# Performance work log

Measured on AMD Instinct MI355X. Metric: run time of the kernel, lower is better.

The kernel has to match this reference:

```python
import jax, jax.numpy as jnp
import numpy as np

B0 = 4
DIM = 128        # d_model / channels
D_INNER = 256    # expand * dim
D_STATE = 16
D_CONV = 4
DT_RANK = 8      # ceil(dim/16)
NSLICES = 16
IMG = (16, 24, 24)
EPS_LN = 1e-5    # nn.LayerNorm default
EPS_CF = 1e-6    # channels_first LayerNorm eps


def setup_inputs() -> dict:
    key = jax.random.key(0)
    ks = jax.random.split(key, 32)
    rn = lambda k, s, sc=1.0: jax.random.normal(k, s, jnp.float32) * sc
    inp = {"x": rn(ks[0], (B0, DIM) + IMG)}
    inp["ln_w"] = jnp.ones((DIM,), jnp.float32)
    inp["ln_b"] = jnp.zeros((DIM,), jnp.float32)
    inp["in_proj_w"] = rn(ks[1], (2 * D_INNER, DIM), 0.05)
    inp["out_proj_w"] = rn(ks[2], (DIM, D_INNER), 0.05)
    for i, sfx in enumerate(["f", "b", "s"]):
        b = 3 + i * 7
        inp[f"conv_w_{sfx}"] = rn(ks[b], (D_INNER, 1, D_CONV), 0.2)
        inp[f"conv_b_{sfx}"] = rn(ks[b + 1], (D_INNER,), 0.02)
        inp[f"xproj_w_{sfx}"] = rn(ks[b + 2], (DT_RANK + 2 * D_STATE, D_INNER), 0.05)
        inp[f"dtproj_w_{sfx}"] = rn(ks[b + 3], (D_INNER, DT_RANK), 0.1)
        inp[f"dtproj_b_{sfx}"] = rn(ks[b + 4], (D_INNER,), 0.1)
        # S4D-real-style init: A in [1, d_state]
        inp[f"A_log_{sfx}"] = jnp.log(jax.random.uniform(ks[b + 5], (D_INNER, D_STATE), jnp.float32, 1.0, 16.0))
        inp[f"D_{sfx}"] = jnp.ones((D_INNER,), jnp.float32)
    inp["nm_w"] = jnp.ones((DIM,), jnp.float32)
    inp["nm_b"] = jnp.zeros((DIM,), jnp.float32)
    return inp


def _mamba_inner(xz, conv_w, conv_b, xproj_w, dtproj_w, dtproj_b, A_log, Dp):
    """mamba_inner_fn_no_out_proj: xz (B, 2*d_inner, L) -> y (B, d_inner, L)."""
    d = conv_w.shape[0]
    x, z = xz[:, :d], xz[:, d:]
    # causal depthwise conv1d
    xc = jax.lax.conv_general_dilated(
        x, conv_w, (1,), [(conv_w.shape[-1] - 1, 0)],
        dimension_numbers=("NCH", "OIH", "NCH"), feature_group_count=d)
    xc = jax.nn.silu(xc + conv_b[None, :, None])
    x_dbl = jnp.einsum("bdl,rd->brl", xc, xproj_w)  # (B, R+2N, L)
    R = dtproj_w.shape[1]
    N = A_log.shape[1]
    dt = jax.nn.softplus(jnp.einsum("brl,dr->bdl", x_dbl[:, :R], dtproj_w) + dtproj_b[None, :, None])
    Bm, Cm = x_dbl[:, R:R + N], x_dbl[:, R + N:]
    A = -jnp.exp(A_log)  # (d, N)
    seq = (jnp.moveaxis(dt, -1, 0), jnp.moveaxis(xc, -1, 0),
           jnp.moveaxis(Bm, -1, 0), jnp.moveaxis(Cm, -1, 0))
    h0 = jnp.zeros((xz.shape[0], d, N), xz.dtype)

    def step(h, t):
        dt_t, u_t, B_t, C_t = t  # (B,d) (B,d) (B,N) (B,N)
        h = h * jnp.exp(dt_t[..., None] * A) + (dt_t * u_t)[..., None] * B_t[:, None, :]
        return h, jnp.einsum("bdn,bn->bd", h, C_t)

    _, ys = jax.lax.scan(step, h0, seq)  # ys: (L, B, d)
    y = jnp.moveaxis(ys, 0, -1) + Dp[None, :, None] * xc
    return y * jax.nn.silu(z)


def reference(x, ln_w, ln_b, in_proj_w, out_proj_w,
              conv_w_f, conv_b_f, xproj_w_f, dtproj_w_f, dtproj_b_f, A_log_f, D_f,
              conv_w_b, conv_b_b, xproj_w_b, dtproj_w_b, dtproj_b_b, A_log_b, D_b,
              conv_w_s, conv_b_s, xproj_w_s, dtproj_w_s, dtproj_b_s, A_log_s, D_s,
              nm_w, nm_b):
    B, C = x.shape[:2]
    img = x.shape[2:]
    L = int(np.prod(img))
    xf = jnp.transpose(x.reshape(B, C, L), (0, 2, 1))  # (B, L, C)
    # MambaLayer.norm (nn.LayerNorm over C)
    mu = xf.mean(-1, keepdims=True)
    var = ((xf - mu) ** 2).mean(-1, keepdims=True)
    xn = (xf - mu) / jnp.sqrt(var + EPS_LN) * ln_w + ln_b
    xz = jnp.einsum("blc,ec->bel", xn, in_proj_w)  # (B, 2*d_inner, L)
    # forward-direction scan
    out_f = _mamba_inner(xz, conv_w_f, conv_b_f, xproj_w_f, dtproj_w_f, dtproj_b_f, A_log_f, D_f)
    # backward-direction scan on flipped sequence, flipped back
    out_bw = jnp.flip(_mamba_inner(jnp.flip(xz, -1), conv_w_b, conv_b_b, xproj_w_b,
                                   dtproj_w_b, dtproj_b_b, A_log_b, D_b), -1)
    # slice-direction: torch chunk(nslices,-1) -> stack(-1) -> flatten(-2)
    ns, Lns = NSLICES, L // NSLICES
    xz_s = jnp.transpose(xz.reshape(B, 2 * D_INNER, ns, Lns), (0, 1, 3, 2)).reshape(B, 2 * D_INNER, L)
    out_s = _mamba_inner(xz_s, conv_w_s, conv_b_s, xproj_w_s, dtproj_w_s, dtproj_b_s, A_log_s, D_s)
    # torch: reshape(B,-1,ns,L//ns).permute(0,1,3,2).flatten(-2)
    out_s = jnp.transpose(out_s.reshape(B, D_INNER, ns, Lns), (0, 1, 3, 2)).reshape(B, D_INNER, L)
    y = jnp.einsum("bdl,cd->blc", out_f + out_bw + out_s, out_proj_w)  # out_proj, no bias
    x_mamba = jnp.transpose(y, (0, 2, 1)).reshape(x.shape) + x  # MambaLayer residual
    # SMBBlock: channels_first LayerNorm + residual
    mu2 = x_mamba.mean(1, keepdims=True)
    var2 = ((x_mamba - mu2) ** 2).mean(1, keepdims=True)
    bc = (C,) + (1,) * len(img)
    normed = nm_w.reshape(bc) * ((x_mamba - mu2) / jnp.sqrt(var2 + EPS_CF)) + nm_b.reshape(bc)
    return x_mamba + normed
```

## Files before the change

kernel.cpp:

```cpp
#include <hip/hip_runtime.h>

#define LSEQ 9216
#define CDIM 128
#define ED   512
#define DI   256
#define NST  16
#define NCH  512
#define CHL  18
#define SEG  32
#define LOG2E 1.44269504f
#define LN2  0.6931471805599453f

#if defined(__has_builtin)
#  if __has_builtin(__builtin_amdgcn_exp2f)
#    define FEXP2(x) __builtin_amdgcn_exp2f(x)
#  endif
#  if __has_builtin(__builtin_amdgcn_logf)
#    define FLOG2(x) __builtin_amdgcn_logf(x)
#  endif
#  if __has_builtin(__builtin_amdgcn_rcpf)
#    define FRCP(x) __builtin_amdgcn_rcpf(x)
#  endif
#endif
#ifndef FEXP2
#  define FEXP2(x) exp2f(x)
#endif
#ifndef FLOG2
#  define FLOG2(x) log2f(x)
#endif
#ifndef FRCP
#  define FRCP(x) (1.f / (x))
#endif

typedef __attribute__((ext_vector_type(8))) short short8v;
typedef __attribute__((ext_vector_type(4))) float float4v;

__device__ __forceinline__ float fsilu(float x) {
  return x * FRCP(1.f + FEXP2(-LOG2E * x));
}
__device__ __forceinline__ float fsoftplus(float x) {
  float sp = FLOG2(1.f + FEXP2(LOG2E * x)) * LN2;
  return (x > 20.f) ? x : sp;
}
__device__ __forceinline__ unsigned short f2bf(float f) {
  union { float f; unsigned u; } v; v.f = f;
  return (unsigned short)((v.u + 0x7FFFu + ((v.u >> 16) & 1u)) >> 16);
}
__device__ __forceinline__ float bf2f(unsigned short u) {
  union { unsigned u; float f; } v; v.u = ((unsigned)u) << 16;
  return v.f;
}
__device__ __forceinline__ int lmap(int p, int mode) {
  if (mode == 0) return p;
  if (mode == 1) return LSEQ - 1 - p;
  return (p & 15) * 576 + (p >> 4);
}

__global__ __launch_bounds__(256) void a2_kernel(
    const float* __restrict__ Af, const float* __restrict__ Ab,
    const float* __restrict__ As, float* __restrict__ A2) {
  int i = blockIdx.x * 256 + threadIdx.x;
  if (i >= 3 * DI * NST) return;
  int dir = i / (DI * NST), j = i % (DI * NST);
  const float* src = (dir == 0) ? Af : ((dir == 1) ? Ab : As);
  A2[i] = -expf(src[j]) * LOG2E;
}

__global__ __launch_bounds__(256) void wcast_kernel(
    const float* __restrict__ src, unsigned short* __restrict__ dst, int n) {
  int i = blockIdx.x * 256 + threadIdx.x;
  if (i < n) dst[i] = f2bf(src[i]);
}

__global__ __launch_bounds__(256) void ln_kernel(
    const float* __restrict__ x, const float* __restrict__ w,
    const float* __restrict__ bb, unsigned short* __restrict__ xn) {
  __shared__ float xt[CDIM][65];
  __shared__ float ps[4][64], pq[4][64];
  __shared__ float mu_s[64], rs_s[64];
  const int b = blockIdx.y, l0 = blockIdx.x * 64, tid = threadIdx.x;
  for (int idx = tid; idx < CDIM * 64; idx += 256) {
    int c = idx >> 6, ll = idx & 63;
    xt[c][ll] = x[((size_t)(b * CDIM + c)) * LSEQ + l0 + ll];
  }
  __syncthreads();
  {
    int ll = tid & 63, grp = tid >> 6;
    float s = 0.f, q = 0.f;
    for (int c = grp * 32; c < grp * 32 + 32; ++c) {
      float v = xt[c][ll]; s += v; q += v * v;
    }
    ps[grp][ll] = s; pq[grp][ll] = q;
  }
  __syncthreads();
  if (tid < 64) {
    float S = ps[0][tid] + ps[1][tid] + ps[2][tid] + ps[3][tid];
    float Q = pq[0][tid] + pq[1][tid] + pq[2][tid] + pq[3][tid];
    float mu = S * (1.f / 128.f);
    float var = Q * (1.f / 128.f) - mu * mu;
    mu_s[tid] = mu;
    rs_s[tid] = rsqrtf(var + 1e-5f);
  }
  __syncthreads();
  for (int idx = tid; idx < 64 * CDIM; idx += 256) {
    int c = idx & 127, ll = idx >> 7;
    float v = (xt[c][ll] - mu_s[ll]) * rs_s[ll] * w[c] + bb[c];
    xn[((size_t)(b * LSEQ + l0 + ll)) * CDIM + c] = f2bf(v);
  }
}

template <bool A_BF16, bool OUT_BF16>
__global__ __launch_bounds__(256) void gemm_mfma(
    const void* __restrict__ Ap, const unsigned short* __restrict__ Wb,
    void* __restrict__ Outp, int N, int K, int ldo) {
  __shared__ __align__(16) unsigned short As[64][40];
  __shared__ __align__(16) unsigned short Bs[128][40];
  const int tid = threadIdx.x;
  const int lane = tid & 63, wid = tid >> 6;
  const int wr = wid >> 1, wc = wid & 1;
  const int m0 = blockIdx.x * 64, n0 = blockIdx.y * 128;
  float4v acc[2][4];
#pragma unroll
  for (int s = 0; s < 2; ++s)
#pragma unroll
    for (int t = 0; t < 4; ++t)
#pragma unroll
      for (int r = 0; r < 4; ++r) acc[s][t][r] = 0.f;

  const int srow = tid >> 2, sslot = tid & 3;
  for (int k0 = 0; k0 < K; k0 += 32) {
    if constexpr (A_BF16) {
      const unsigned short* A = (const unsigned short*)Ap;
      *(short8v*)&As[srow][sslot * 8] =
          *(const short8v*)&A[(size_t)(m0 + srow) * K + k0 + sslot * 8];
    } else {
      const float* A = (const float*)Ap;
      const float4* src = (const float4*)&A[(size_t)(m0 + srow) * K + k0 + sslot * 8];
      float4 f0 = src[0], f1 = src[1];
      short8v v;
      v[0] = (short)f2bf(f0.x); v[1] = (short)f2bf(f0.y);
      v[2] = (short)f2bf(f0.z); v[3] = (short)f2bf(f0.w);
      v[4] = (short)f2bf(f1.x); v[5] = (short)f2bf(f1.y);
      v[6] = (short)f2bf(f1.z); v[7] = (short)f2bf(f1.w);
      *(short8v*)&As[srow][sslot * 8] = v;
    }
#pragma unroll
    for (int i = 0; i < 2; ++i) {
      int row = i * 64 + srow;
      int n = n0 + row;
      short8v v;
      if (n < N) {
        v = *(const short8v*)&Wb[(size_t)n * K + k0 + sslot * 8];
      } else {
#pragma unroll
        for (int q = 0; q < 8; ++q) v[q] = 0;
      }
      *(short8v*)&Bs[row][sslot * 8] = v;
    }
    __syncthreads();
    const int kk = (lane >> 4) * 8;
    const int mr = wr * 32 + (lane & 15);
    const int nr = wc * 64 + (lane & 15);
    short8v a_frag[2], b_frag[4];
#pragma unroll
    for (int s = 0; s < 2; ++s)
      a_frag[s] = *(const short8v*)&As[mr + s * 16][kk];
#pragma unroll
    for (int t = 0; t < 4; ++t)
      b_frag[t] = *(const short8v*)&Bs[nr + t * 16][kk];
#pragma unroll
    for (int s = 0; s < 2; ++s)
#pragma unroll
      for (int t = 0; t < 4; ++t)
        acc[s][t] = __builtin_amdgcn_mfma_f32_16x16x32_bf16(
            a_frag[s], b_frag[t], acc[s][t], 0, 0, 0);
    __syncthreads();
  }
  const int rbase = (lane >> 4) * 4;
  const int cbase = lane & 15;
#pragma unroll
  for (int s = 0; s < 2; ++s)
#pragma unroll
    for (int t = 0; t < 4; ++t) {
      int n = n0 + wc * 64 + t * 16 + cbase;
      if (n < N) {
#pragma unroll
        for (int r = 0; r < 4; ++r) {
          int m = m0 + wr * 32 + s * 16 + rbase + r;
          if constexpr (OUT_BF16)
            ((unsigned short*)Outp)[(size_t)m * ldo + n] = f2bf(acc[s][t][r]);
          else
            ((float*)Outp)[(size_t)m * ldo + n] = acc[s][t][r];
        }
      }
    }
}

__global__ __launch_bounds__(256) void gemm_out_final(
    const unsigned short* __restrict__ yf, const unsigned short* __restrict__ yb,
    const unsigned short* __restrict__ ys, const unsigned short* __restrict__ Wb,
    const float* __restrict__ x, const float* __restrict__ nmw,
    const float* __restrict__ nmb, float* __restrict__ out) {
  __shared__ __align__(16) unsigned short As[64][40];
  __shared__ __align__(16) unsigned short Bs[128][40];
  __shared__ float yt[64][129];
  __shared__ float ps[4][64], pq[4][64], mu_s[64], rs_s[64];
  const int tid = threadIdx.x;
  const int lane = tid & 63, wid = tid >> 6;
  const int wr = wid >> 1, wc = wid & 1;
  const int m0 = blockIdx.x * 64;
  const int b = blockIdx.x / 144, l0 = (blockIdx.x % 144) * 64;
  float4v acc[2][4];
#pragma unroll
  for (int s = 0; s < 2; ++s)
#pragma unroll
    for (int t = 0; t < 4; ++t)
#pragma unroll
      for (int r = 0; r < 4; ++r) acc[s][t][r] = 0.f;

  const int srow = tid >> 2, sslot = tid & 3;
  for (int k0 = 0; k0 < 256; k0 += 32) {
    {
      size_t base = (size_t)(m0 + srow) * DI + k0 + sslot * 8;
      short8v vf = *(const short8v*)&yf[base];
      short8v vb = *(const short8v*)&yb[base];
      short8v vs = *(const short8v*)&ys[base];
      short8v v;
#pragma unroll
      for (int q = 0; q < 8; ++q) {
        float f = bf2f((unsigned short)vf[q]) + bf2f((unsigned short)vb[q]) +
                  bf2f((unsigned short)vs[q]);
        v[q] = (short)f2bf(f);
      }
      *(short8v*)&As[srow][sslot * 8] = v;
    }
#pragma unroll
    for (int i = 0; i < 2; ++i) {
      int row = i * 64 + srow;
      *(short8v*)&Bs[row][sslot * 8] =
          *(const short8v*)&Wb[(size_t)row * 256 + k0 + sslot * 8];
    }
    __syncthreads();
    const int kk = (lane >> 4) * 8;
    const int mr = wr * 32 + (lane & 15);
    const int nr = wc * 64 + (lane & 15);
    short8v a_frag[2], b_frag[4];
#pragma unroll
    for (int s = 0; s < 2; ++s)
      a_frag[s] = *(const short8v*)&As[mr + s * 16][kk];
#pragma unroll
    for (int t = 0; t < 4; ++t)
      b_frag[t] = *(const short8v*)&Bs[nr + t * 16][kk];
#pragma unroll
    for (int s = 0; s < 2; ++s)
#pragma unroll
      for (int t = 0; t < 4; ++t)
        acc[s][t] = __builtin_amdgcn_mfma_f32_16x16x32_bf16(
            a_frag[s], b_frag[t], acc[s][t], 0, 0, 0);
    __syncthreads();
  }
  const int rbase = (lane >> 4) * 4;
  const int cbase = lane & 15;
#pragma unroll
  for (int s = 0; s < 2; ++s)
#pragma unroll
    for (int t = 0; t < 4; ++t) {
      int cc = wc * 64 + t * 16 + cbase;
#pragma unroll
      for (int r = 0; r < 4; ++r)
        yt[wr * 32 + s * 16 + rbase + r][cc] = acc[s][t][r];
    }
  __syncthreads();
  for (int idx = tid; idx < CDIM * 64; idx += 256) {
    int c = idx >> 6, ll = idx & 63;
    yt[ll][c] += x[((size_t)(b * CDIM + c)) * LSEQ + l0 + ll];
  }
  __syncthreads();
  {
    int ll = tid & 63, grp = tid >> 6;
    float s = 0.f, q = 0.f;
    for (int c = grp * 32; c < grp * 32 + 32; ++c) {
      float v = yt[ll][c]; s += v; q += v * v;
    }
    ps[grp][ll] = s; pq[grp][ll] = q;
  }
  __syncthreads();
  if (tid < 64) {
    float S = ps[0][tid] + ps[1][tid] + ps[2][tid] + ps[3][tid];
    float Q = pq[0][tid] + pq[1][tid] + pq[2][tid] + pq[3][tid];
    float mu = S * (1.f / 128.f);
    float var = Q * (1.f / 128.f) - mu * mu;
    mu_s[tid] = mu;
    rs_s[tid] = rsqrtf(var + 1e-6f);
  }
  __syncthreads();
  for (int idx = tid; idx < CDIM * 64; idx += 256) {
    int c = idx >> 6, ll = idx & 63;
    float v = yt[ll][c];
    out[((size_t)(b * CDIM + c)) * LSEQ + l0 + ll] =
        v + nmw[c] * (v - mu_s[ll]) * rs_s[ll] + nmb[c];
  }
}

template <int MODE>
__global__ __launch_bounds__(256) void conv_kernel(
    const unsigned short* __restrict__ xz, const float* __restrict__ cw,
    const float* __restrict__ cb, unsigned short* __restrict__ xc) {
  __shared__ float xs[67][64];
  const int p0 = blockIdx.x * 64, d0 = blockIdx.y * 64, b = blockIdx.z;
  const int tid = threadIdx.x;
  for (int idx = tid; idx < 67 * 32; idx += 256) {
    int pp = idx >> 5, dd2 = idx & 31;
    int q = p0 + pp - 3;
    float v0 = 0.f, v1 = 0.f;
    if (q >= 0) {
      int l = lmap(q, MODE);
      unsigned uu = *(const unsigned*)&xz[((size_t)b * LSEQ + l) * ED + d0 + dd2 * 2];
      union { unsigned u; float f; } a, c;
      a.u = (uu & 0xFFFFu) << 16;
      c.u = uu & 0xFFFF0000u;
      v0 = a.f; v1 = c.f;
    }
    xs[pp][dd2 * 2] = v0;
    xs[pp][dd2 * 2 + 1] = v1;
  }
  __syncthreads();
  const int dd = tid & 63, pg = tid >> 6;
  const int d = d0 + dd;
  const float w0 = cw[d * 4 + 0], w1 = cw[d * 4 + 1];
  const float w2 = cw[d * 4 + 2], w3 = cw[d * 4 + 3];
  const float bias = cb[d];
  for (int pp = pg * 16; pp < pg * 16 + 16; ++pp) {
    float acc = bias + w0 * xs[pp][dd] + w1 * xs[pp + 1][dd] +
                w2 * xs[pp + 2][dd] + w3 * xs[pp + 3][dd];
    xc[((size_t)b * LSEQ + p0 + pp) * DI + d] = f2bf(fsilu(acc));
  }
}

__global__ __launch_bounds__(256, 8) void scan_p1(
    const unsigned short* __restrict__ xc, const float* __restrict__ xdbl,
    const float* __restrict__ A2, const float* __restrict__ dtw,
    const float* __restrict__ dtbias, unsigned short* __restrict__ hout,
    float* __restrict__ dts) {
  __shared__ __align__(16) float Xl[CHL][24];
  const int c = blockIdx.x, b = blockIdx.y, d = threadIdx.x;
  const int p0 = c * CHL;
  for (int idx = d; idx < CHL * 24; idx += 256) {
    int pr = idx / 24, r = idx % 24;
    Xl[pr][r] = xdbl[((size_t)b * LSEQ + p0 + pr) * 40 + r];
  }
  float a2[NST], h[NST], dw[8];
  {
    const float4* A2v = (const float4*)(A2 + d * NST);
#pragma unroll
    for (int q = 0; q < 4; ++q) {
      float4 t = A2v[q];
      a2[q * 4 + 0] = t.x; a2[q * 4 + 1] = t.y;
      a2[q * 4 + 2] = t.z; a2[q * 4 + 3] = t.w;
    }
    const float4* Wv = (const float4*)(dtw + d * 8);
    float4 w0 = Wv[0], w1 = Wv[1];
    dw[0] = w0.x; dw[1] = w0.y; dw[2] = w0.z; dw[3] = w0.w;
    dw[4] = w1.x; dw[5] = w1.y; dw[6] = w1.z; dw[7] = w1.w;
  }
#pragma unroll
  for (int n = 0; n < NST; ++n) h[n] = 0.f;
  const float dbias = dtbias[d];
  float dtsum = 0.f;
  const unsigned short* up = xc + ((size_t)b * LSEQ + p0) * DI + d;
  __syncthreads();
  for (int pr = 0; pr < CHL; ++pr) {
    const float u = bf2f(*up); up += DI;
    const float4* Xr = (const float4*)Xl[pr];
    float4 x0 = Xr[0], x1 = Xr[1];
    float raw = dbias;
    raw = fmaf(dw[0], x0.x, raw); raw = fmaf(dw[1], x0.y, raw);
    raw = fmaf(dw[2], x0.z, raw); raw = fmaf(dw[3], x0.w, raw);
    raw = fmaf(dw[4], x1.x, raw); raw = fmaf(dw[5], x1.y, raw);
    raw = fmaf(dw[6], x1.z, raw); raw = fmaf(dw[7], x1.w, raw);
    const float dtv = fsoftplus(raw);
    const float dtu = dtv * u;
    dtsum += dtv;
    float4 b0 = Xr[2], b1 = Xr[3], b2 = Xr[4], b3 = Xr[5];
    const float Bv[16] = {b0.x, b0.y, b0.z, b0.w, b1.x, b1.y, b1.z, b1.w,
                          b2.x, b2.y, b2.z, b2.w, b3.x, b3.y, b3.z, b3.w};
#pragma unroll
    for (int n = 0; n < NST; ++n) {
      float a = FEXP2(dtv * a2[n]);
      h[n] = fmaf(h[n], a, dtu * Bv[n]);
    }
  }
  unsigned short* hb = hout + (((size_t)c * 4 + b) * DI + d) * NST;
  uint4 pk0, pk1;
  pk0.x = ((unsigned)f2bf(h[1]) << 16) | f2bf(h[0]);
  pk0.y = ((unsigned)f2bf(h[3]) << 16) | f2bf(h[2]);
  pk0.z = ((unsigned)f2bf(h[5]) << 16) | f2bf(h[4]);
  pk0.w = ((unsigned)f2bf(h[7]) << 16) | f2bf(h[6]);
  pk1.x = ((unsigned)f2bf(h[9]) << 16) | f2bf(h[8]);
  pk1.y = ((unsigned)f2bf(h[11]) << 16) | f2bf(h[10]);
  pk1.z = ((unsigned)f2bf(h[13]) << 16) | f2bf(h[12]);
  pk1.w = ((unsigned)f2bf(h[15]) << 16) | f2bf(h[14]);
  *(uint4*)hb = pk0;
  *(uint4*)(hb + 8) = pk1;
  dts[((size_t)c * 4 + b) * DI + d] = dtsum;
}

__global__ __launch_bounds__(256) void scan_p2a(
    unsigned short* __restrict__ hbuf, const float* __restrict__ dts,
    const float* __restrict__ A2, float* __restrict__ cumdts,
    float* __restrict__ segH, float* __restrict__ segdts) {
  const int s = blockIdx.x >> 4;
  const int rest = ((blockIdx.x & 15) << 8) + threadIdx.x;
  const int b = blockIdx.y;
  const int d = rest >> 4;
  const float a2 = A2[rest];
  const int c0 = s * SEG;
  float h = 0.f, cum = 0.f;
  float nh = bf2f(hbuf[((size_t)(c0 * 4 + b) << 12) + rest]);
  float nd = dts[(size_t)(c0 * 4 + b) * DI + d];
  for (int c = c0; c < c0 + SEG; ++c) {
    const float tmp = nh, dcur = nd;
    if (c + 1 < c0 + SEG) {
      nh = bf2f(hbuf[((size_t)((c + 1) * 4 + b) << 12) + rest]);
      nd = dts[(size_t)((c + 1) * 4 + b) * DI + d];
    }
    if ((rest & 15) == 0) cumdts[(size_t)(c * 4 + b) * DI + d] = cum;
    cum += dcur;
    hbuf[((size_t)(c * 4 + b) << 12) + rest] = f2bf(h);
    h = fmaf(FEXP2(dcur * a2), h, tmp);
  }
  segH[((size_t)(s * 4 + b) << 12) + rest] = h;
  if ((rest & 15) == 0) segdts[(size_t)(s * 4 + b) * DI + d] = cum;
}

__global__ __launch_bounds__(256) void scan_p2b(
    const float* __restrict__ segH, const float* __restrict__ segdts,
    const float* __restrict__ A2, float* __restrict__ segcarry) {
  const int g = blockIdx.x * 256 + threadIdx.x;
  const int b = g >> 12;
  const int rest = g & 4095;
  const int d = rest >> 4;
  const float a2 = A2[rest];
  float carry = 0.f;
#pragma unroll
  for (int s = 0; s < 16; ++s) {
    segcarry[((size_t)(s * 4 + b) << 12) + rest] = carry;
    const float decay = FEXP2(segdts[(size_t)(s * 4 + b) * DI + d] * a2);
    carry = fmaf(decay, carry, segH[((size_t)(s * 4 + b) << 12) + rest]);
  }
}

template <int MODE>
__global__ __launch_bounds__(256, 8) void scan_p3(
    const unsigned short* __restrict__ xc, const float* __restrict__ xdbl,
    const unsigned short* __restrict__ xz, const float* __restrict__ A2,
    const float* __restrict__ dtw, const float* __restrict__ dtbias,
    const unsigned short* __restrict__ hinit, const float* __restrict__ cumdts,
    const float* __restrict__ segcarry, const float* __restrict__ Dp,
    unsigned short* __restrict__ ybuf) {
  __shared__ __align__(16) float Xl[CHL][40];
  const int c = blockIdx.x, b = blockIdx.y, d = threadIdx.x;
  const int p0 = c * CHL;
  for (int idx = d; idx < CHL * 40; idx += 256) {
    int pr = idx / 40, r = idx % 40;
    Xl[pr][r] = xdbl[((size_t)b * LSEQ + p0 + pr) * 40 + r];
  }
  float a2[NST], h[NST], dw[8];
  {
    const float4* A2v = (const float4*)(A2 + d * NST);
#pragma unroll
    for (int q = 0; q < 4; ++q) {
      float4 t = A2v[q];
      a2[q * 4 + 0] = t.x; a2[q * 4 + 1] = t.y;
      a2[q * 4 + 2] = t.z; a2[q * 4 + 3] = t.w;
    }
    const uint4* Hv = (const uint4*)(hinit + (((size_t)c * 4 + b) * DI + d) * NST);
    uint4 pa = Hv[0], pb = Hv[1];
    const unsigned pw[8] = {pa.x, pa.y, pa.z, pa.w, pb.x, pb.y, pb.z, pb.w};
#pragma unroll
    for (int j = 0; j < 8; ++j) {
      union { unsigned u; float f; } lo, hi;
      lo.u = (pw[j] & 0xFFFFu) << 16;
      hi.u = pw[j] & 0xFFFF0000u;
      h[2 * j] = lo.f; h[2 * j + 1] = hi.f;
    }
    const float cum = cumdts[((size_t)c * 4 + b) * DI + d];
    const float4* SC = (const float4*)(segcarry +
        (((size_t)(c / SEG) * 4 + b) << 12) + d * NST);
#pragma unroll
    for (int q = 0; q < 4; ++q) {
      float4 sc = SC[q];
      const float scv[4] = {sc.x, sc.y, sc.z, sc.w};
#pragma unroll
      for (int r = 0; r < 4; ++r) {
        int n = q * 4 + r;
        h[n] = fmaf(FEXP2(a2[n] * cum), scv[r], h[n]);
      }
    }
    const float4* Wv = (const float4*)(dtw + d * 8);
    float4 w0 = Wv[0], w1 = Wv[1];
    dw[0] = w0.x; dw[1] = w0.y; dw[2] = w0.z; dw[3] = w0.w;
    dw[4] = w1.x; dw[5] = w1.y; dw[6] = w1.z; dw[7] = w1.w;
  }
  const float dbias = dtbias[d];
  const float Dv = Dp[d];

  const unsigned short* up = xc + ((size_t)b * LSEQ + p0) * DI + d;
  const unsigned short* zp;
  unsigned short* op;
  ptrdiff_t zstride, ostride;
  if (MODE == 0) {
    zp = xz + ((size_t)b * LSEQ + p0) * ED + DI + d;              zstride = ED;
    op = ybuf + ((size_t)b * LSEQ + p0) * DI + d;                 ostride = DI;
  } else if (MODE == 1) {
    zp = xz + ((size_t)b * LSEQ + (LSEQ - 1 - p0)) * ED + DI + d; zstride = -(ptrdiff_t)ED;
    op = ybuf + ((size_t)b * LSEQ + (LSEQ - 1 - p0)) * DI + d;    ostride = -(ptrdiff_t)DI;
  } else {
    zp = nullptr; zstride = 0;
    const int lo0 = (p0 % 576) * 16 + p0 / 576;
    op = ybuf + ((size_t)b * LSEQ + lo0) * DI + d;                ostride = 16 * DI;
  }
  __syncthreads();
  for (int pr = 0; pr < CHL; ++pr) {
    const float u = bf2f(*up); up += DI;
    const float4* Xr = (const float4*)Xl[pr];
    float4 x0 = Xr[0], x1 = Xr[1];
    float raw = dbias;
    raw = fmaf(dw[0], x0.x, raw); raw = fmaf(dw[1], x0.y, raw);
    raw = fmaf(dw[2], x0.z, raw); raw = fmaf(dw[3], x0.w, raw);
    raw = fmaf(dw[4], x1.x, raw); raw = fmaf(dw[5], x1.y, raw);
    raw = fmaf(dw[6], x1.z, raw); raw = fmaf(dw[7], x1.w, raw);
    const float dtv = fsoftplus(raw);
    const float dtu = dtv * u;
    float4 b0 = Xr[2], b1 = Xr[3], b2 = Xr[4], b3 = Xr[5];
    float4 c0 = Xr[6], c1 = Xr[7], c2 = Xr[8], c3 = Xr[9];
    const float Bv[16] = {b0.x, b0.y, b0.z, b0.w, b1.x, b1.y, b1.z, b1.w,
                          b2.x, b2.y, b2.z, b2.w, b3.x, b3.y, b3.z, b3.w};
    const float Cv[16] = {c0.x, c0.y, c0.z, c0.w, c1.x, c1.y, c1.z, c1.w,
                          c2.x, c2.y, c2.z, c2.w, c3.x, c3.y, c3.z, c3.w};
    float y0 = Dv * u, y1 = 0.f;
#pragma unroll
    for (int n = 0; n < NST; ++n) {
      float a = FEXP2(dtv * a2[n]);
      h[n] = fmaf(h[n], a, dtu * Bv[n]);
      if (n & 1) y1 = fmaf(h[n], Cv[n], y1);
      else       y0 = fmaf(h[n], Cv[n], y0);
    }
    float z;
    if (MODE == 2) {
      const int p = p0 + pr;
      const int lz = (p & 15) * 576 + (p >> 4);
      z = bf2f(xz[((size_t)b * LSEQ + lz) * ED + DI + d]);
    } else {
      z = bf2f(*zp); zp += zstride;
    }
    *op = f2bf((y0 + y1) * fsilu(z));
    op += ostride;
  }
}

extern "C" void kernel_launch(void* const* d_in, const int* in_sizes, int n_in,
                              void* d_out, int out_size, void* d_ws, size_t ws_size,
                              hipStream_t stream) {
  (void)in_sizes; (void)n_in; (void)out_size;
  const float* x         = (const float*)d_in[0];
  const float* ln_w      = (const float*)d_in[1];
  const float* ln_b      = (const float*)d_in[2];
  const float* in_proj_w = (const float*)d_in[3];
  const float* out_projw = (const float*)d_in[4];
  const float* conv_w[3] = {(const float*)d_in[5],  (const float*)d_in[12], (const float*)d_in[19]};
  const float* conv_b[3] = {(const float*)d_in[6],  (const float*)d_in[13], (const float*)d_in[20]};
  const float* xproj[3]  = {(const float*)d_in[7],  (const float*)d_in[14], (const float*)d_in[21]};
  const float* dtw[3]    = {(const float*)d_in[8],  (const float*)d_in[15], (const float*)d_in[22]};
  const float* dtb[3]    = {(const float*)d_in[9],  (const float*)d_in[16], (const float*)d_in[23]};
  const float* alog[3]   = {(const float*)d_in[10], (const float*)d_in[17], (const float*)d_in[24]};
  const float* Dvec[3]   = {(const float*)d_in[11], (const float*)d_in[18], (const float*)d_in[25]};
  const float* nm_w      = (const float*)d_in[26];
  const float* nm_b      = (const float*)d_in[27];

  float* ws = (float*)d_ws;
  unsigned short* xn_us   = (unsigned short*)(ws);
  unsigned short* xz_us   = (unsigned short*)(ws + 2359296);
  unsigned short* xc_us   = (unsigned short*)(ws + 11796480);
  float* xdbl   = ws + 16515072;
  unsigned short* yf_us   = (unsigned short*)(ws + 17989632);
  unsigned short* yb_us   = (unsigned short*)(ws + 22708224);
  unsigned short* ys_us   = (unsigned short*)(ws + 27426816);
  float* A2     = ws + 32145408;
  unsigned short* wb = (unsigned short*)(ws + 32157696);
  unsigned short* hout_us = (unsigned short*)(ws + 32223232);
  float* dts      = ws + 36417536;
  float* cumdts   = ws + 36941824;
  float* segH     = ws + 37466112;
  float* segdts   = ws + 37728256;
  float* segcarry = ws + 37744640;
  if (ws_size < (size_t)38006784 * sizeof(float)) return;

  unsigned short* wb_in  = wb;
  unsigned short* wb_xp0 = wb + 65536;
  unsigned short* wb_xp1 = wb + 75776;
  unsigned short* wb_xp2 = wb + 86016;
  unsigned short* wb_out = wb + 96256;
  unsigned short* wb_xp[3] = {wb_xp0, wb_xp1, wb_xp2};
  unsigned short* ybuf[3] = {yf_us, yb_us, ys_us};

  a2_kernel<<<48, 256, 0, stream>>>(alog[0], alog[1], alog[2], A2);
  wcast_kernel<<<256, 256, 0, stream>>>(in_proj_w, wb_in, 65536);
  wcast_kernel<<<40, 256, 0, stream>>>(xproj[0], wb_xp0, 10240);
  wcast_kernel<<<40, 256, 0, stream>>>(xproj[1], wb_xp1, 10240);
  wcast_kernel<<<40, 256, 0, stream>>>(xproj[2], wb_xp2, 10240);
  wcast_kernel<<<128, 256, 0, stream>>>(out_projw, wb_out, 32768);

  ln_kernel<<<dim3(LSEQ / 64, 4), 256, 0, stream>>>(x, ln_w, ln_b, xn_us);
  gemm_mfma<true, true><<<dim3(576, 4), 256, 0, stream>>>(xn_us, wb_in, xz_us, 512, 128, 512);

  for (int dir = 0; dir < 3; ++dir) {
    if (dir == 0)
      conv_kernel<0><<<dim3(LSEQ / 64, 4, 4), 256, 0, stream>>>(xz_us, conv_w[0], conv_b[0], xc_us);
    else if (dir == 1)
      conv_kernel<1><<<dim3(LSEQ / 64, 4, 4), 256, 0, stream>>>(xz_us, conv_w[1], conv_b[1], xc_us);
    else
      conv_kernel<2><<<dim3(LSEQ / 64, 4, 4), 256, 0, stream>>>(xz_us, conv_w[2], conv_b[2], xc_us);

    gemm_mfma<true, false><<<dim3(576, 1), 256, 0, stream>>>(xc_us, wb_xp[dir], xdbl, 40, 256, 40);

    const float* A2d = A2 + dir * 4096;
    dim3 sg(NCH, 4);
    scan_p1<<<sg, 256, 0, stream>>>(xc_us, xdbl, A2d, dtw[dir], dtb[dir], hout_us, dts);
    scan_p2a<<<dim3(256, 4), 256, 0, stream>>>(hout_us, dts, A2d, cumdts, segH, segdts);
    scan_p2b<<<64, 256, 0, stream>>>(segH, segdts, A2d, segcarry);

    if (dir == 0)
      scan_p3<0><<<sg, 256, 0, stream>>>(xc_us, xdbl, xz_us, A2d, dtw[0], dtb[0],
                                         hout_us, cumdts, segcarry, Dvec[0], ybuf[0]);
    else if (dir == 1)
      scan_p3<1><<<sg, 256, 0, stream>>>(xc_us, xdbl, xz_us, A2d, dtw[1], dtb[1],
                                         hout_us, cumdts, segcarry, Dvec[1], ybuf[1]);
    else
      scan_p3<2><<<sg, 256, 0, stream>>>(xc_us, xdbl, xz_us, A2d, dtw[2], dtb[2],
                                         hout_us, cumdts, segcarry, Dvec[2], ybuf[2]);
  }
  gemm_out_final<<<576, 256, 0, stream>>>(yf_us, yb_us, ys_us, wb_out, x,
                                          nm_w, nm_b, (float*)d_out);
}
```

Measured before the change: 442.4 us.

## Split scan state dimension across two threads per channel in scan kernels

```diff
diff --git a/kernel.cpp b/kernel.cpp
--- a/kernel.cpp
+++ b/kernel.cpp
@@ -343,28 +343,27 @@
     const float* __restrict__ dtbias, unsigned short* __restrict__ hout,
     float* __restrict__ dts) {
   __shared__ __align__(16) float Xl[CHL][24];
-  const int c = blockIdx.x, b = blockIdx.y, d = threadIdx.x;
+  const int c = blockIdx.x, b = blockIdx.y;
+  const int d = (blockIdx.z << 7) + (threadIdx.x >> 1);
+  const int s = threadIdx.x & 1;
   const int p0 = c * CHL;
-  for (int idx = d; idx < CHL * 24; idx += 256) {
+  for (int idx = threadIdx.x; idx < CHL * 24; idx += 256) {
     int pr = idx / 24, r = idx % 24;
     Xl[pr][r] = xdbl[((size_t)b * LSEQ + p0 + pr) * 40 + r];
   }
-  float a2[NST], h[NST], dw[8];
+  float a2[8], h[8], dw[8];
   {
-    const float4* A2v = (const float4*)(A2 + d * NST);
-#pragma unroll
-    for (int q = 0; q < 4; ++q) {
-      float4 t = A2v[q];
-      a2[q * 4 + 0] = t.x; a2[q * 4 + 1] = t.y;
-      a2[q * 4 + 2] = t.z; a2[q * 4 + 3] = t.w;
-    }
+    const float4* A2v = (const float4*)(A2 + d * NST + s * 8);
+    float4 t0 = A2v[0], t1 = A2v[1];
+    a2[0] = t0.x; a2[1] = t0.y; a2[2] = t0.z; a2[3] = t0.w;
+    a2[4] = t1.x; a2[5] = t1.y; a2[6] = t1.z; a2[7] = t1.w;
     const float4* Wv = (const float4*)(dtw + d * 8);
     float4 w0 = Wv[0], w1 = Wv[1];
     dw[0] = w0.x; dw[1] = w0.y; dw[2] = w0.z; dw[3] = w0.w;
     dw[4] = w1.x; dw[5] = w1.y; dw[6] = w1.z; dw[7] = w1.w;
   }
 #pragma unroll
-  for (int n = 0; n < NST; ++n) h[n] = 0.f;
+  for (int n = 0; n < 8; ++n) h[n] = 0.f;
   const float dbias = dtbias[d];
   float dtsum = 0.f;
   const unsigned short* up = xc + ((size_t)b * LSEQ + p0) * DI + d;
@@ -381,28 +380,22 @@
     const float dtv = fsoftplus(raw);
     const float dtu = dtv * u;
     dtsum += dtv;
-    float4 b0 = Xr[2], b1 = Xr[3], b2 = Xr[4], b3 = Xr[5];
-    const float Bv[16] = {b0.x, b0.y, b0.z, b0.w, b1.x, b1.y, b1.z, b1.w,
-                          b2.x, b2.y, b2.z, b2.w, b3.x, b3.y, b3.z, b3.w};
-#pragma unroll
-    for (int n = 0; n < NST; ++n) {
+    float4 b0 = Xr[2 + 2 * s], b1 = Xr[3 + 2 * s];
+    const float Bv[8] = {b0.x, b0.y, b0.z, b0.w, b1.x, b1.y, b1.z, b1.w};
+#pragma unroll
+    for (int n = 0; n < 8; ++n) {
       float a = FEXP2(dtv * a2[n]);
       h[n] = fmaf(h[n], a, dtu * Bv[n]);
     }
   }
-  unsigned short* hb = hout + (((size_t)c * 4 + b) * DI + d) * NST;
-  uint4 pk0, pk1;
-  pk0.x = ((unsigned)f2bf(h[1]) << 16) | f2bf(h[0]);
-  pk0.y = ((unsigned)f2bf(h[3]) << 16) | f2bf(h[2]);
-  pk0.z = ((unsigned)f2bf(h[5]) << 16) | f2bf(h[4]);
-  pk0.w = ((unsigned)f2bf(h[7]) << 16) | f2bf(h[6]);
-  pk1.x = ((unsigned)f2bf(h[9]) << 16) | f2bf(h[8]);
-  pk1.y = ((unsigned)f2bf(h[11]) << 16) | f2bf(h[10]);
-  pk1.z = ((unsigned)f2bf(h[13]) << 16) | f2bf(h[12]);
-  pk1.w = ((unsigned)f2bf(h[15]) << 16) | f2bf(h[14]);
-  *(uint4*)hb = pk0;
-  *(uint4*)(hb + 8) = pk1;
-  dts[((size_t)c * 4 + b) * DI + d] = dtsum;
+  unsigned short* hb = hout + (((size_t)c * 4 + b) * DI + d) * NST + s * 8;
+  uint4 pk;
+  pk.x = ((unsigned)f2bf(h[1]) << 16) | f2bf(h[0]);
+  pk.y = ((unsigned)f2bf(h[3]) << 16) | f2bf(h[2]);
+  pk.z = ((unsigned)f2bf(h[5]) << 16) | f2bf(h[4]);
+  pk.w = ((unsigned)f2bf(h[7]) << 16) | f2bf(h[6]);
+  *(uint4*)hb = pk;
+  if (s == 0) dts[((size_t)c * 4 + b) * DI + d] = dtsum;
 }
 
 __global__ __launch_bounds__(256) void scan_p2a(
@@ -459,26 +452,25 @@
     const float* __restrict__ segcarry, const float* __restrict__ Dp,
     unsigned short* __restrict__ ybuf) {
   __shared__ __align__(16) float Xl[CHL][40];
-  const int c = blockIdx.x, b = blockIdx.y, d = threadIdx.x;
+  const int c = blockIdx.x, b = blockIdx.y;
+  const int d = (blockIdx.z << 7) + (threadIdx.x >> 1);
+  const int s = threadIdx.x & 1;
   const int p0 = c * CHL;
-  for (int idx = d; idx < CHL * 40; idx += 256) {
+  for (int idx = threadIdx.x; idx < CHL * 40; idx += 256) {
     int pr = idx / 40, r = idx % 40;
     Xl[pr][r] = xdbl[((size_t)b * LSEQ + p0 + pr) * 40 + r];
   }
-  float a2[NST], h[NST], dw[8];
+  float a2[8], h[8], dw[8];
   {
-    const float4* A2v = (const float4*)(A2 + d * NST);
-#pragma unroll
-    for (int q = 0; q < 4; ++q) {
-      float4 t = A2v[q];
-      a2[q * 4 + 0] = t.x; a2[q * 4 + 1] = t.y;
-      a2[q * 4 + 2] = t.z; a2[q * 4 + 3] = t.w;
-    }
-    const uint4* Hv = (const uint4*)(hinit + (((size_t)c * 4 + b) * DI + d) * NST);
-    uint4 pa = Hv[0], pb = Hv[1];
-    const unsigned pw[8] = {pa.x, pa.y, pa.z, pa.w, pb.x, pb.y, pb.z, pb.w};
-#pragma unroll
-    for (int j = 0; j < 8; ++j) {
+    const float4* A2v = (const float4*)(A2 + d * NST + s * 8);
+    float4 t0 = A2v[0], t1 = A2v[1];
+    a2[0] = t0.x; a2[1] = t0.y; a2[2] = t0.z; a2[3] = t0.w;
+    a2[4] = t1.x; a2[5] = t1.y; a2[6] = t1.z; a2[7] = t1.w;
+    const uint4* Hv = (const uint4*)(hinit + (((size_t)c * 4 + b) * DI + d) * NST + s * 8);
+    uint4 pa = Hv[0];
+    const unsigned pw[4] = {pa.x, pa.y, pa.z, pa.w};
+#pragma unroll
+    for (int j = 0; j < 4; ++j) {
       union { unsigned u; float f; } lo, hi;
       lo.u = (pw[j] & 0xFFFFu) << 16;
       hi.u = pw[j] & 0xFFFF0000u;
@@ -486,17 +478,12 @@
     }
     const float cum = cumdts[((size_t)c * 4 + b) * DI + d];
     const float4* SC = (const float4*)(segcarry +
-        (((size_t)(c / SEG) * 4 + b) << 12) + d * NST);
-#pragma unroll
-    for (int q = 0; q < 4; ++q) {
-      float4 sc = SC[q];
-      const float scv[4] = {sc.x, sc.y, sc.z, sc.w};
-#pragma unroll
-      for (int r = 0; r < 4; ++r) {
-        int n = q * 4 + r;
-        h[n] = fmaf(FEXP2(a2[n] * cum), scv[r], h[n]);
-      }
-    }
+        (((size_t)(c / SEG) * 4 + b) << 12) + d * NST + s * 8);
+    float4 sc0 = SC[0], sc1 = SC[1];
+    const float scv[8] = {sc0.x, sc0.y, sc0.z, sc0.w, sc1.x, sc1.y, sc1.z, sc1.w};
+#pragma unroll
+    for (int n = 0; n < 8; ++n)
+      h[n] = fmaf(FEXP2(a2[n] * cum), scv[n], h[n]);
     const float4* Wv = (const float4*)(dtw + d * 8);
     float4 w0 = Wv[0], w1 = Wv[1];
     dw[0] = w0.x; dw[1] = w0.y; dw[2] = w0.z; dw[3] = w0.w;
@@ -532,29 +519,30 @@
     raw = fmaf(dw[6], x1.z, raw); raw = fmaf(dw[7], x1.w, raw);
     const float dtv = fsoftplus(raw);
     const float dtu = dtv * u;
-    float4 b0 = Xr[2], b1 = Xr[3], b2 = Xr[4], b3 = Xr[5];
-    float4 c0 = Xr[6], c1 = Xr[7], c2 = Xr[8], c3 = Xr[9];
-    const float Bv[16] = {b0.x, b0.y, b0.z, b0.w, b1.x, b1.y, b1.z, b1.w,
-                          b2.x, b2.y, b2.z, b2.w, b3.x, b3.y, b3.z, b3.w};
-    const float Cv[16] = {c0.x, c0.y, c0.z, c0.w, c1.x, c1.y, c1.z, c1.w,
-                          c2.x, c2.y, c2.z, c2.w, c3.x, c3.y, c3.z, c3.w};
-    float y0 = Dv * u, y1 = 0.f;
-#pragma unroll
-    for (int n = 0; n < NST; ++n) {
+    float4 b0 = Xr[2 + 2 * s], b1 = Xr[3 + 2 * s];
+    float4 c0 = Xr[6 + 2 * s], c1 = Xr[7 + 2 * s];
+    const float Bv[8] = {b0.x, b0.y, b0.z, b0.w, b1.x, b1.y, b1.z, b1.w};
+    const float Cv[8] = {c0.x, c0.y, c0.z, c0.w, c1.x, c1.y, c1.z, c1.w};
+    float y = (s == 0) ? Dv * u : 0.f;
+#pragma unroll
+    for (int n = 0; n < 8; ++n) {
       float a = FEXP2(dtv * a2[n]);
       h[n] = fmaf(h[n], a, dtu * Bv[n]);
-      if (n & 1) y1 = fmaf(h[n], Cv[n], y1);
-      else       y0 = fmaf(h[n], Cv[n], y0);
-    }
-    float z;
-    if (MODE == 2) {
-      const int p = p0 + pr;
-      const int lz = (p & 15) * 576 + (p >> 4);
-      z = bf2f(xz[((size_t)b * LSEQ + lz) * ED + DI + d]);
-    } else {
-      z = bf2f(*zp); zp += zstride;
-    }
-    *op = f2bf((y0 + y1) * fsilu(z));
+      y = fmaf(h[n], Cv[n], y);
+    }
+    y += __shfl_xor(y, 1);
+    if (s == 0) {
+      float z;
+      if (MODE == 2) {
+        const int p = p0 + pr;
+        const int lz = (p & 15) * 576 + (p >> 4);
+        z = bf2f(xz[((size_t)b * LSEQ + lz) * ED + DI + d]);
+      } else {
+        z = bf2f(*zp);
+      }
+      *op = f2bf(y * fsilu(z));
+    }
+    if (MODE != 2) zp += zstride;
     op += ostride;
   }
 }
@@ -625,7 +613,7 @@
     gemm_mfma<true, false><<<dim3(576, 1), 256, 0, stream>>>(xc_us, wb_xp[dir], xdbl, 40, 256, 40);
 
     const float* A2d = A2 + dir * 4096;
-    dim3 sg(NCH, 4);
+    dim3 sg(NCH, 4, 2);
     scan_p1<<<sg, 256, 0, stream>>>(xc_us, xdbl, A2d, dtw[dir], dtb[dir], hout_us, dts);
     scan_p2a<<<dim3(256, 4), 256, 0, stream>>>(hout_us, dts, A2d, cumdts, segH, segdts);
     scan_p2b<<<64, 256, 0, stream>>>(segH, segdts, A2d, segcarry);
```

After: 438.2 us. No clear change (-0.9%).
